# Optimization experiments

Measured on AMD Instinct MI355X. Metric: run time of the kernel, lower is better.

The kernel has to match this reference:

```python
import jax, jax.numpy as jnp
import numpy as np

TIME_STEPS = 8

def setup_inputs() -> dict:
    key = jax.random.key(0)
    feature_matrix = jax.random.normal(key, (64, 1, 1000, 128), dtype=jnp.float32)
    return {"feature_matrix": feature_matrix}

def reference(feature_matrix):
    # squeeze channel -> (B, F, Bd)
    x = jnp.squeeze(feature_matrix, axis=1)
    min_val = jnp.min(x, axis=(1, 2), keepdims=True)
    max_val = jnp.max(x, axis=(1, 2), keepdims=True)
    norm = TIME_STEPS * (x - min_val) / (max_val - min_val)  # values in [0, 8]
    # The torch loop (mask = v > 0; store; v[mask] -= 1) is exactly equivalent to
    # mask_t = (norm > t) for t = 0..TIME_STEPS-1, since once v <= 0 it never
    # becomes positive again. Vectorize over the time axis in one pass.
    t = jnp.arange(TIME_STEPS, dtype=norm.dtype)  # (T,)
    spikes = (norm[..., None] > t).astype(jnp.float32)  # (B, F, Bd, T)
    # torch.randperm shuffle of time axis; use a fixed permutation for determinism
    perm = jax.random.permutation(jax.random.key(1), TIME_STEPS)
    spikes = spikes[..., perm]
    return spikes[:, None]  # (B, 1, F, Bd, T)
```

## Files before the change

### kernel.cpp

```cpp
#include <hip/hip_runtime.h>
#include <cstdint>
#include <cstddef>


#define JAX_PARTITIONABLE 1

struct TF2 { uint32_t a, b; };

constexpr uint32_t rotl32(uint32_t x, int d) { return (x << d) | (x >> (32 - d)); }

constexpr TF2 threefry2x32(uint32_t k0, uint32_t k1, uint32_t x0, uint32_t x1) {
  const uint32_t ks2 = k0 ^ k1 ^ 0x1BD11BDAu;
  const int R0[4] = {13, 15, 26, 6};
  const int R1[4] = {17, 29, 16, 24};
  x0 += k0; x1 += k1;
  for (int i = 0; i < 4; ++i) { x0 += x1; x1 = rotl32(x1, R0[i]); x1 ^= x0; }
  x0 += k1; x1 += ks2 + 1u;
  for (int i = 0; i < 4; ++i) { x0 += x1; x1 = rotl32(x1, R1[i]); x1 ^= x0; }
  x0 += ks2; x1 += k0 + 2u;
  for (int i = 0; i < 4; ++i) { x0 += x1; x1 = rotl32(x1, R0[i]); x1 ^= x0; }
  x0 += k0; x1 += k1 + 3u;
  for (int i = 0; i < 4; ++i) { x0 += x1; x1 = rotl32(x1, R1[i]); x1 ^= x0; }
  x0 += k1; x1 += ks2 + 4u;
  for (int i = 0; i < 4; ++i) { x0 += x1; x1 = rotl32(x1, R0[i]); x1 ^= x0; }
  x0 += ks2; x1 += k0 + 5u;
  return TF2{x0, x1};
}

struct Perm { int p[8]; };

constexpr Perm compute_perm() {
  uint32_t sk0 = 0, sk1 = 0;
  uint32_t bits[8] = {};
#if JAX_PARTITIONABLE
  {
    TF2 s = threefry2x32(0u, 1u, 0u, 1u);
    sk0 = s.a; sk1 = s.b;
  }
  for (int i = 0; i < 8; ++i) {
    TF2 r = threefry2x32(sk0, sk1, 0u, (uint32_t)i);
    bits[i] = r.a ^ r.b;
  }
#else
  {
    TF2 l0 = threefry2x32(0u, 1u, 0u, 2u);
    TF2 l1 = threefry2x32(0u, 1u, 1u, 3u);
    sk0 = l0.b; sk1 = l1.b;
  }
  for (int i = 0; i < 4; ++i) {
    TF2 r = threefry2x32(sk0, sk1, (uint32_t)i, (uint32_t)(i + 4));
    bits[i] = r.a; bits[i + 4] = r.b;
  }
#endif
  Perm perm = {{0, 1, 2, 3, 4, 5, 6, 7}};
  for (int i = 1; i < 8; ++i) {
    uint32_t kb = bits[i]; int kv = perm.p[i];
    int j = i - 1;
    while (j >= 0 && bits[j] > kb) { bits[j + 1] = bits[j]; perm.p[j + 1] = perm.p[j]; --j; }
    bits[j + 1] = kb; perm.p[j + 1] = kv;
  }
  return perm;
}

constexpr Perm PERM = compute_perm();

static constexpr int B = 64;
static constexpr int PER_BATCH = 1000 * 128;
static constexpr int PER_BATCH_F4 = PER_BATCH / 4;
static constexpr int MM_BLOCKS_PER_BATCH = 16;
static constexpr int MM_F4_PER_BLOCK = PER_BATCH_F4 / MM_BLOCKS_PER_BATCH;
static constexpr int ENC_BLOCKS = (B * PER_BATCH_F4) / 256;

__device__ inline uint32_t f2key(float f) {
  uint32_t u = __float_as_uint(f);
  return (u & 0x80000000u) ? ~u : (u | 0x80000000u);
}
__device__ inline float key2f(uint32_t k) {
  uint32_t u = (k & 0x80000000u) ? (k & 0x7FFFFFFFu) : ~k;
  return __uint_as_float(u);
}

__global__ __launch_bounds__(128) void init_keys(uint32_t* keys) {
  int i = threadIdx.x;
  keys[i] = (i & 1) ? 0u : 0xFFFFFFFFu;
}

__global__ __launch_bounds__(256) void minmax_kernel(const float4* __restrict__ in,
                                                     uint32_t* __restrict__ keys) {
  const int batch = blockIdx.x >> 4;
  const int sub = blockIdx.x & 15;
  const float4* bp = in + (size_t)batch * PER_BATCH_F4;
  float mn = INFINITY, mx = -INFINITY;
  const int end = (sub + 1) * MM_F4_PER_BLOCK;
  for (int i = sub * MM_F4_PER_BLOCK + threadIdx.x; i < end; i += 256) {
    float4 v = bp[i];
    mn = fminf(mn, fminf(fminf(v.x, v.y), fminf(v.z, v.w)));
    mx = fmaxf(mx, fmaxf(fmaxf(v.x, v.y), fmaxf(v.z, v.w)));
  }
  #pragma unroll
  for (int off = 32; off > 0; off >>= 1) {
    mn = fminf(mn, __shfl_down(mn, off));
    mx = fmaxf(mx, __shfl_down(mx, off));
  }
  __shared__ float smn[4], smx[4];
  const int wave = threadIdx.x >> 6, lane = threadIdx.x & 63;
  if (lane == 0) { smn[wave] = mn; smx[wave] = mx; }
  __syncthreads();
  if (threadIdx.x == 0) {
    mn = fminf(fminf(smn[0], smn[1]), fminf(smn[2], smn[3]));
    mx = fmaxf(fmaxf(smx[0], smx[1]), fmaxf(smx[2], smx[3]));
    atomicMin(&keys[2 * batch], f2key(mn));
    atomicMax(&keys[2 * batch + 1], f2key(mx));
  }
}

__global__ __launch_bounds__(256) void encode_kernel(const float4* __restrict__ in,
                                                     float4* __restrict__ out,
                                                     const uint32_t* __restrict__ keys) {
  const int t4 = blockIdx.x * 256 + threadIdx.x;
  const int batch = blockIdx.x / 125;
  const float mn = key2f(keys[2 * batch]);
  const float mx = key2f(keys[2 * batch + 1]);
  const float rng = mx - mn;

  const float4 x = in[t4];
  float n[4];
  n[0] = (8.0f * (x.x - mn)) / rng;
  n[1] = (8.0f * (x.y - mn)) / rng;
  n[2] = (8.0f * (x.z - mn)) / rng;
  n[3] = (8.0f * (x.w - mn)) / rng;

  constexpr float TH[8] = {
    (float)PERM.p[0], (float)PERM.p[1], (float)PERM.p[2], (float)PERM.p[3],
    (float)PERM.p[4], (float)PERM.p[5], (float)PERM.p[6], (float)PERM.p[7]
  };

  float4 o[8];
  #pragma unroll
  for (int e = 0; e < 4; ++e) {
    o[2 * e + 0].x = n[e] > TH[0] ? 1.0f : 0.0f;
    o[2 * e + 0].y = n[e] > TH[1] ? 1.0f : 0.0f;
    o[2 * e + 0].z = n[e] > TH[2] ? 1.0f : 0.0f;
    o[2 * e + 0].w = n[e] > TH[3] ? 1.0f : 0.0f;
    o[2 * e + 1].x = n[e] > TH[4] ? 1.0f : 0.0f;
    o[2 * e + 1].y = n[e] > TH[5] ? 1.0f : 0.0f;
    o[2 * e + 1].z = n[e] > TH[6] ? 1.0f : 0.0f;
    o[2 * e + 1].w = n[e] > TH[7] ? 1.0f : 0.0f;
  }

  float4* op = out + (size_t)t4 * 8;
  #pragma unroll
  for (int k = 0; k < 8; ++k) op[k] = o[k];
}

extern "C" void kernel_launch(void* const* d_in, const int* in_sizes, int n_in,
                              void* d_out, int out_size, void* d_ws, size_t ws_size,
                              hipStream_t stream) {
  const float4* in = (const float4*)d_in[0];
  float4* out = (float4*)d_out;
  uint32_t* keys = (uint32_t*)d_ws;

  hipLaunchKernelGGL(init_keys, dim3(1), dim3(128), 0, stream, keys);
  hipLaunchKernelGGL(minmax_kernel, dim3(B * MM_BLOCKS_PER_BATCH), dim3(256), 0, stream,
                     in, keys);
  hipLaunchKernelGGL(encode_kernel, dim3(ENC_BLOCKS), dim3(256), 0, stream,
                     in, out, keys);
}
```

Baseline: 327.0 us.

## Remap encode kernel for coalesced float4 output with nontemporal stores

The encode kernel now has each thread write one float4 of output per iteration, with consecutive threads writing consecutive float4s. Before, each thread wrote 8 contiguous float4s, so writes within a wave were strided. Each thread handles one half of an element's 8 time steps (even or odd lane), reading scalar inputs that neighbouring lanes share. Stores become nontemporal to avoid polluting the cache with the large output. The cost is redundant input loads (each element is read twice) and an extra division per element. The JAX_PARTITIONABLE switch is also removed, keeping only the partitionable threefry path.

Measured after the change: 285.0 us. -12.8%, faster.

```diff
diff --git a/kernel.cpp b/kernel.cpp
--- a/kernel.cpp
+++ b/kernel.cpp
@@ -3,7 +3,7 @@
 #include <cstddef>
 
 
-#define JAX_PARTITIONABLE 1
+typedef float f32x4 __attribute__((ext_vector_type(4)));
 
 struct TF2 { uint32_t a, b; };
 
@@ -30,28 +30,13 @@
 struct Perm { int p[8]; };
 
 constexpr Perm compute_perm() {
-  uint32_t sk0 = 0, sk1 = 0;
+  TF2 s = threefry2x32(0u, 1u, 0u, 1u);
+  uint32_t sk0 = s.a, sk1 = s.b;
   uint32_t bits[8] = {};
-#if JAX_PARTITIONABLE
-  {
-    TF2 s = threefry2x32(0u, 1u, 0u, 1u);
-    sk0 = s.a; sk1 = s.b;
-  }
   for (int i = 0; i < 8; ++i) {
     TF2 r = threefry2x32(sk0, sk1, 0u, (uint32_t)i);
     bits[i] = r.a ^ r.b;
   }
-#else
-  {
-    TF2 l0 = threefry2x32(0u, 1u, 0u, 2u);
-    TF2 l1 = threefry2x32(0u, 1u, 1u, 3u);
-    sk0 = l0.b; sk1 = l1.b;
-  }
-  for (int i = 0; i < 4; ++i) {
-    TF2 r = threefry2x32(sk0, sk1, (uint32_t)i, (uint32_t)(i + 4));
-    bits[i] = r.a; bits[i + 4] = r.b;
-  }
-#endif
   Perm perm = {{0, 1, 2, 3, 4, 5, 6, 7}};
   for (int i = 1; i < 8; ++i) {
     uint32_t kb = bits[i]; int kv = perm.p[i];
@@ -69,7 +54,10 @@
 static constexpr int PER_BATCH_F4 = PER_BATCH / 4;
 static constexpr int MM_BLOCKS_PER_BATCH = 16;
 static constexpr int MM_F4_PER_BLOCK = PER_BATCH_F4 / MM_BLOCKS_PER_BATCH;
-static constexpr int ENC_BLOCKS = (B * PER_BATCH_F4) / 256;
+
+static constexpr int ENC_OUT4_PER_BLOCK = 2048;
+static constexpr int ENC_BLOCKS = 16384000 / ENC_OUT4_PER_BLOCK;
+static constexpr int ENC_BLOCKS_PER_BATCH = 125;
 
 __device__ inline uint32_t f2key(float f) {
   uint32_t u = __float_as_uint(f);
@@ -114,55 +102,45 @@
   }
 }
 
-__global__ __launch_bounds__(256) void encode_kernel(const float4* __restrict__ in,
-                                                     float4* __restrict__ out,
+__global__ __launch_bounds__(256) void encode_kernel(const float* __restrict__ in,
+                                                     f32x4* __restrict__ out,
                                                      const uint32_t* __restrict__ keys) {
-  const int t4 = blockIdx.x * 256 + threadIdx.x;
-  const int batch = blockIdx.x / 125;
+  const int batch = blockIdx.x / ENC_BLOCKS_PER_BATCH;
   const float mn = key2f(keys[2 * batch]);
   const float mx = key2f(keys[2 * batch + 1]);
   const float rng = mx - mn;
 
-  const float4 x = in[t4];
-  float n[4];
-  n[0] = (8.0f * (x.x - mn)) / rng;
-  n[1] = (8.0f * (x.y - mn)) / rng;
-  n[2] = (8.0f * (x.z - mn)) / rng;
-  n[3] = (8.0f * (x.w - mn)) / rng;
+  const int p = (threadIdx.x & 1) * 4;
+  const float th0 = (float)PERM.p[p + 0];
+  const float th1 = (float)PERM.p[p + 1];
+  const float th2 = (float)PERM.p[p + 2];
+  const float th3 = (float)PERM.p[p + 3];
 
-  constexpr float TH[8] = {
-    (float)PERM.p[0], (float)PERM.p[1], (float)PERM.p[2], (float)PERM.p[3],
-    (float)PERM.p[4], (float)PERM.p[5], (float)PERM.p[6], (float)PERM.p[7]
-  };
-
-  float4 o[8];
+  const int out4_base = blockIdx.x * ENC_OUT4_PER_BLOCK + threadIdx.x;
   #pragma unroll
-  for (int e = 0; e < 4; ++e) {
-    o[2 * e + 0].x = n[e] > TH[0] ? 1.0f : 0.0f;
-    o[2 * e + 0].y = n[e] > TH[1] ? 1.0f : 0.0f;
-    o[2 * e + 0].z = n[e] > TH[2] ? 1.0f : 0.0f;
-    o[2 * e + 0].w = n[e] > TH[3] ? 1.0f : 0.0f;
-    o[2 * e + 1].x = n[e] > TH[4] ? 1.0f : 0.0f;
-    o[2 * e + 1].y = n[e] > TH[5] ? 1.0f : 0.0f;
-    o[2 * e + 1].z = n[e] > TH[6] ? 1.0f : 0.0f;
-    o[2 * e + 1].w = n[e] > TH[7] ? 1.0f : 0.0f;
+  for (int k = 0; k < 8; ++k) {
+    const int o4 = out4_base + k * 256;
+    const float x = in[o4 >> 1];
+    const float n = (8.0f * (x - mn)) / rng;
+    f32x4 o;
+    o.x = n > th0 ? 1.0f : 0.0f;
+    o.y = n > th1 ? 1.0f : 0.0f;
+    o.z = n > th2 ? 1.0f : 0.0f;
+    o.w = n > th3 ? 1.0f : 0.0f;
+    __builtin_nontemporal_store(o, &out[o4]);
   }
-
-  float4* op = out + (size_t)t4 * 8;
-  #pragma unroll
-  for (int k = 0; k < 8; ++k) op[k] = o[k];
 }
 
 extern "C" void kernel_launch(void* const* d_in, const int* in_sizes, int n_in,
                               void* d_out, int out_size, void* d_ws, size_t ws_size,
                               hipStream_t stream) {
-  const float4* in = (const float4*)d_in[0];
-  float4* out = (float4*)d_out;
+  const float* in = (const float*)d_in[0];
+  f32x4* out = (f32x4*)d_out;
   uint32_t* keys = (uint32_t*)d_ws;
 
   hipLaunchKernelGGL(init_keys, dim3(1), dim3(128), 0, stream, keys);
   hipLaunchKernelGGL(minmax_kernel, dim3(B * MM_BLOCKS_PER_BATCH), dim3(256), 0, stream,
-                     in, keys);
+                     (const float4*)in, keys);
   hipLaunchKernelGGL(encode_kernel, dim3(ENC_BLOCKS), dim3(256), 0, stream,
                      in, out, keys);
 }
```
